# Kernel optimization log

Hardware: AMD Instinct MI355X
Metric: run time of the kernel (lower is better)

Reference implementation:

```python
import jax, jax.numpy as jnp
import numpy as np

BETA = 10.0


def _read_buffer(alpha, B, s_b, pop):
    # alpha: [b], B: [b,S,H], s_b: [b,S]. Closed form of the saturating
    # sequential read: cumsum after i steps = min(prefix_sum(s_b)_i, alpha),
    # so weight_i = min(P_i, alpha) - min(P_{i-1}, alpha).
    P = jnp.cumsum(s_b, axis=1)
    Pc = jnp.minimum(P, alpha[:, None])
    w = Pc - jnp.concatenate([jnp.zeros_like(Pc[:, :1]), Pc[:, :-1]], axis=1)
    vec = jnp.einsum('bs,bsh->bh', w, B)
    return vec, (s_b - w if pop else s_b)


def _read_stack(alpha, V, s, pop):
    # V: [M,b,H], s: [M,b]; smaller index = closer to stack top (unused slots
    # above the top have s==0 and contribute nothing).
    P = jnp.cumsum(s, axis=0)                 # [M,b]
    a = alpha[None, :]
    Pc1 = jnp.minimum(P, a)                   # saturate at alpha (first read)
    Pc2 = jnp.minimum(P, 1.0 + a)             # saturate at 1+alpha (both reads)
    z = jnp.zeros_like(P[:1])
    w1 = Pc1 - jnp.concatenate([z, Pc1[:-1]], axis=0)
    wt = Pc2 - jnp.concatenate([z, Pc2[:-1]], axis=0)
    w2 = wt - w1
    v1 = jnp.einsum('mb,mbh->bh', w1, V)
    v2 = jnp.einsum('mb,mbh->bh', w2, V)
    return v1, v2, (s - wt if pop else s)


def _forward(x, emb_table, lstm_wih, lstm_whh, lstm_bih, lstm_bhh,
             alpha_w, alpha_b, tree_left_w, tree_left_b, tree_right_w,
             tree_right_b, l0_w, l0_b, l1_w, l1_b, l2_w, l2_b):
    b, S = x.shape
    H = emb_table.shape[1]
    time = 2 * S
    M = 1 + 2 * time                          # max stack depth
    B = emb_table[x]                          # [b,S,H]
    s_b0 = (x > 0).astype(jnp.float32)
    V0 = jnp.zeros((M, b, H), jnp.float32)    # initial sentinel at M-1 (zeros)
    s0 = jnp.zeros((M, b), jnp.float32)
    h0 = jnp.zeros((b, H), jnp.float32)
    c0 = jnp.zeros((b, H), jnp.float32)
    ones_b = jnp.ones((b,), jnp.float32)

    def step(carry, t):
        s_b, V, s, h, c = carry
        n = 1 + 2 * t                         # current number of stack items
        x_b, _ = _read_buffer(ones_b, B, s_b, False)
        x1, x2, _ = _read_stack(ones_b, V, s, False)
        xt = jnp.concatenate([x_b, x1, x2], axis=1)
        # LSTMCell (torch gate order i,f,g,o)
        g = xt @ lstm_wih.T + lstm_bih + h @ lstm_whh.T + lstm_bhh
        gi, gf, gg, go = jnp.split(g, 4, axis=1)
        c = jax.nn.sigmoid(gf) * c + jax.nn.sigmoid(gi) * jnp.tanh(gg)
        h = jax.nn.sigmoid(go) * jnp.tanh(c)
        alphas = jax.nn.softmax(BETA * (h @ alpha_w.T + alpha_b), axis=1)
        a_r, a_s = alphas[:, 0], alphas[:, 1]
        # reduce: pop ~2 items, treeLSTM, push result with strength alpha_r
        r1, r2, s = _read_stack(a_r, V, s, True)
        tg = r1 @ tree_left_w.T + tree_left_b + r2 @ tree_right_w.T + tree_right_b
        ta, ti, tf1, tf2, to = jnp.split(tg, 5, axis=1)
        ct = jnp.tanh(ta) * jax.nn.sigmoid(ti) + jax.nn.sigmoid(tf1) * r1 + jax.nn.sigmoid(tf2) * r2
        ht = jax.nn.sigmoid(to) * jnp.tanh(ct)
        idx = M - (n + 1)
        V = V.at[idx].set(ht)
        s = s.at[idx].set(a_r)
        # shift: pop from buffer with strength alpha_s, push onto stack
        buf, s_b = _read_buffer(a_s, B, s_b, True)
        idx2 = M - (n + 2)
        V = V.at[idx2].set(buf)
        s = s.at[idx2].set(a_s)
        return (s_b, V, s, h, c), None

    carry, _ = jax.lax.scan(jax.checkpoint(step), (s_b0, V0, s0, h0, c0),
                            jnp.arange(time))
    s_b, V, s, h, c = carry
    x1, _, _ = _read_stack(ones_b, V, s, False)
    # MLP head
    y = jax.nn.relu(x1 @ l0_w.T + l0_b)
    y = jax.nn.relu(y @ l1_w.T + l1_b)
    return y @ l2_w.T + l2_b


def setup_inputs() -> dict:
    key = jax.random.key(0)
    ks = jax.random.split(key, 12)
    b, S, H, V, MLP, C = 64, 48, 256, 50257, 1024, 3
    sc = 0.05
    return {
        'x': jax.random.randint(ks[0], (b, S), 0, V, dtype=jnp.int32).astype(jnp.int64),
        'emb_table': jax.random.normal(ks[1], (V, H), jnp.float32) * sc,
        'lstm_wih': jax.random.normal(ks[2], (4 * H, 3 * H), jnp.float32) * sc,
        'lstm_whh': jax.random.normal(ks[3], (4 * H, H), jnp.float32) * sc,
        'lstm_bih': jnp.zeros((4 * H,), jnp.float32),
        'lstm_bhh': jnp.zeros((4 * H,), jnp.float32),
        'alpha_w': jax.random.normal(ks[4], (2, H), jnp.float32) * sc,
        'alpha_b': jnp.zeros((2,), jnp.float32),
        'tree_left_w': jax.random.normal(ks[5], (5 * H, H), jnp.float32) * sc,
        'tree_left_b': jnp.zeros((5 * H,), jnp.float32),
        'tree_right_w': jax.random.normal(ks[6], (5 * H, H), jnp.float32) * sc,
        'tree_right_b': jnp.zeros((5 * H,), jnp.float32),
        'l0_w': jax.random.normal(ks[7], (MLP, H), jnp.float32) * sc,
        'l0_b': jnp.zeros((MLP,), jnp.float32),
        'l1_w': jax.random.normal(ks[8], (MLP, MLP), jnp.float32) * sc,
        'l1_b': jnp.zeros((MLP,), jnp.float32),
        'l2_w': jax.random.normal(ks[9], (C, MLP), jnp.float32) * sc,
        'l2_b': jnp.zeros((C,), jnp.float32),
    }


def reference(x, emb_table, lstm_wih, lstm_whh, lstm_bih, lstm_bhh, alpha_w,
              alpha_b, tree_left_w, tree_left_b, tree_right_w, tree_right_b,
              l0_w, l0_b, l1_w, l1_b, l2_w, l2_b):
    return _forward(x, emb_table, lstm_wih, lstm_whh, lstm_bih, lstm_bhh,
                    alpha_w, alpha_b, tree_left_w, tree_left_b, tree_right_w,
                    tree_right_b, l0_w, l0_b, l1_w, l1_b, l2_w, l2_b)
```

## Files before the change

kernel.cpp:

```cpp
#include <hip/hip_runtime.h>
#include <math.h>

#define NBLK 512
#define NTHR 512

typedef float vf4 __attribute__((ext_vector_type(4)));

namespace spinn {

constexpr int Ss = 48, Hh = 256, TT = 96, Mm = 193, H3 = 768, MLPD = 1024;

__device__ __forceinline__ float sigf(float x) { return 1.0f / (1.0f + expf(-x)); }

#define FMA4(acc, a, b)                         \
    {                                           \
        acc.x = fmaf((a).x, (b).x, acc.x);      \
        acc.y = fmaf((a).y, (b).y, acc.y);      \
        acc.z = fmaf((a).z, (b).z, acc.z);      \
        acc.w = fmaf((a).w, (b).w, acc.w);      \
    }

__device__ __forceinline__ void st_co(float* p, float v) {
    asm volatile("global_store_dword %0, %1, off sc0 sc1" :: "v"(p), "v"(v) : "memory");
}
__device__ __forceinline__ void ld_co_v4_1(const vf4* p0, vf4& r0) {
    asm volatile("global_load_dwordx4 %0, %1, off sc0 sc1\n\t"
                 "s_waitcnt vmcnt(0)"
                 : "=&v"(r0) : "v"(p0) : "memory");
}
__device__ __forceinline__ void ld_co_f1x4(const float* p0, const float* p1, const float* p2,
                                           const float* p3, float& r0, float& r1, float& r2, float& r3) {
    asm volatile("global_load_dword %0, %4, off sc0 sc1\n\t"
                 "global_load_dword %1, %5, off sc0 sc1\n\t"
                 "global_load_dword %2, %6, off sc0 sc1\n\t"
                 "global_load_dword %3, %7, off sc0 sc1\n\t"
                 "s_waitcnt vmcnt(0)"
                 : "=&v"(r0), "=&v"(r1), "=&v"(r2), "=&v"(r3)
                 : "v"(p0), "v"(p1), "v"(p2), "v"(p3) : "memory");
}
__device__ __forceinline__ unsigned ld_co_u32(const unsigned* p) {
    unsigned r;
    asm volatile("global_load_dword %0, %1, off sc0 sc1\n\t"
                 "s_waitcnt vmcnt(0)"
                 : "=&v"(r) : "v"(p) : "memory");
    return r;
}

__device__ __forceinline__ void gbar(unsigned* cnt, unsigned tgt) {
    asm volatile("s_waitcnt vmcnt(0)" ::: "memory");
    __syncthreads();
    if (threadIdx.x == 0) {
        unsigned one = 1u;
        asm volatile("global_atomic_add %0, %1, off" :: "v"(cnt), "v"(one) : "memory");
        while (ld_co_u32(cnt) < tgt) __builtin_amdgcn_s_sleep(1);
    }
    __syncthreads();
}

__device__ __forceinline__ float wave_iscan(float v, int lane) {
    #pragma unroll
    for (int off = 1; off < 64; off <<= 1) {
        float u = __shfl_up(v, off, 64);
        if (lane >= off) v += u;
    }
    return v;
}
__device__ __forceinline__ float wred64(float v) {
    #pragma unroll
    for (int off = 1; off < 64; off <<= 1) v += __shfl_xor(v, off, 64);
    return v;
}
__device__ __forceinline__ float wred_ms(float v) {
    v += __shfl_xor(v, 16, 64);
    v += __shfl_xor(v, 32, 64);
    return v;
}

}

using namespace spinn;

__global__ void __launch_bounds__(NTHR, 2) spinn_kernel(
    const int* __restrict__ x, const float* __restrict__ emb,
    const float* __restrict__ wih, const float* __restrict__ whh,
    const float* __restrict__ bih, const float* __restrict__ bhh,
    const float* __restrict__ aw, const float* __restrict__ ab,
    const float* __restrict__ tlw, const float* __restrict__ tlb,
    const float* __restrict__ trw, const float* __restrict__ trb,
    const float* __restrict__ l0w, const float* __restrict__ l0b,
    const float* __restrict__ l1w, const float* __restrict__ l1b,
    const float* __restrict__ l2w, const float* __restrict__ l2b,
    float* __restrict__ out, float* __restrict__ wsf, unsigned* __restrict__ bar)
{
    const int tid  = threadIdx.x;
    const int bid  = blockIdx.x;
    const int ep   = bid >> 4;
    const int q    = bid & 15;
    const int db   = q * 16;
    const int e0   = ep * 2;
    const int wave = tid >> 6;
    const int lane = tid & 63;
    const int ms   = lane >> 4;
    const int dl   = lane & 15;

    unsigned* cnt = bar + ep * 32;
    unsigned barnum = 0;

    float* XTg = wsf;
    float* Hbg = XTg + 64 * H3;
    float* R1g = Hbg + 64 * Hh;
    float* R2g = R1g + 64 * Hh;
    float* Y0g = R2g + 64 * Hh;
    float* Y1g = Y0g + 64 * MLPD;

    __shared__ float s_V[2 * 196 * 16];
    __shared__ float s_B[2 * Ss * 16];
    __shared__ float s_xt[2 * H3];
    __shared__ float s_h[2 * 256];
    __shared__ float s_c[32];
    __shared__ float s_g[128];
    __shared__ float s_tg[160];
    __shared__ float s_r1[2 * 256], s_r2[2 * 256];
    __shared__ float s_s[2 * 208];
    __shared__ float sw1[2 * 208], sw2[2 * 208];
    __shared__ float pw1[2 * 208], pw2[2 * 208];
    __shared__ float s_sb[2 * Ss], s_wb[2 * Ss], s_wbe[2 * Ss];
    __shared__ float s_bias[64];
    __shared__ float s_tbias[80];

    float* s_y = s_V;

    {
        if (tid < 384) {
            int el = tid / 192, r = tid % 192;
            int s = r >> 2, j = r & 3;
            int tok = x[(e0 + el) * Ss + s];
            ((vf4*)s_B)[el * 192 + s * 4 + j] = ((const vf4*)emb)[(size_t)tok * 64 + q * 4 + j];
        }
        if (tid < 2 * Ss) {
            int el = tid / Ss, s = tid % Ss;
            s_sb[tid] = (x[(e0 + el) * Ss + s] > 0) ? 1.0f : 0.0f;
        }
        for (int i = tid; i < 2 * 208; i += NTHR) s_s[i] = 0.0f;
        for (int i = tid; i < 2 * 256; i += NTHR) s_h[i] = 0.0f;
        if (tid < 32) s_c[tid] = 0.0f;
        if (tid < 64) {
            int row = (tid >> 4) * Hh + db + (tid & 15);
            s_bias[tid] = bih[row] + bhh[row];
        }
        if (tid < 80) {
            int row = (tid >> 4) * Hh + db + (tid & 15);
            s_tbias[tid] = tlb[row] + trb[row];
        }
        for (int i = tid; i < 2 * 196 * 16; i += NTHR) s_V[i] = 0.0f;
        __syncthreads();
        if (wave < 2) {
            int el = wave;
            float sbv = (lane < Ss) ? s_sb[el * Ss + lane] : 0.0f;
            float P = wave_iscan(sbv, lane);
            float wbe = fminf(P, 1.0f) - fminf(P - sbv, 1.0f);
            if (lane < Ss) s_wbe[el * Ss + lane] = wbe;
            float axb = 0.0f;
            #pragma unroll
            for (int j = 0; j < 12; j++) {
                int s = ms * 12 + j;
                axb = fmaf(s_wbe[el * Ss + s], s_B[el * 768 + s * 16 + dl], axb);
            }
            axb = wred_ms(axb);
            if (lane < 16) {
                float* xte = XTg + (size_t)(e0 + el) * H3;
                st_co(xte + db + dl, axb);
                st_co(xte + 256 + db + dl, 0.0f);
                st_co(xte + 512 + db + dl, 0.0f);
            }
        }
    }
    gbar(cnt, ++barnum * 16);

    for (int t = 0; t < TT; t++) {
        const int idx  = 191 - 2 * t;
        const int idx2 = idx - 1;

        {
            if (tid < 384) {
                int el = tid / 192, r = tid % 192;
                vf4 v;
                ld_co_v4_1((const vf4*)XTg + (size_t)(e0 + el) * 192 + r, v);
                ((vf4*)s_xt)[el * 192 + r] = v;
            }
            __syncthreads();
            const vf4* sxt4 = (const vf4*)s_xt;
            const vf4* sh4  = (const vf4*)s_h;
            vf4 xa0 = sxt4[lane], xa1 = sxt4[64 + lane], xa2 = sxt4[128 + lane];
            vf4 xb0 = sxt4[192 + lane], xb1 = sxt4[256 + lane], xb2 = sxt4[320 + lane];
            vf4 ha = sh4[lane], hb = sh4[64 + lane];
            #pragma unroll 2
            for (int p = 0; p < 8; p++) {
                int r = wave * 8 + p;
                int row = ((r >> 4) << 8) + db + (r & 15);
                const vf4* w  = (const vf4*)wih + (size_t)row * 192;
                const vf4* wh = (const vf4*)whh + (size_t)row * 64;
                vf4 w0 = w[lane], w1 = w[64 + lane], w2 = w[128 + lane], w3 = wh[lane];
                vf4 aa = {0.f, 0.f, 0.f, 0.f}, ab_ = {0.f, 0.f, 0.f, 0.f};
                FMA4(aa, w0, xa0); FMA4(aa, w1, xa1); FMA4(aa, w2, xa2); FMA4(aa, w3, ha);
                FMA4(ab_, w0, xb0); FMA4(ab_, w1, xb1); FMA4(ab_, w2, xb2); FMA4(ab_, w3, hb);
                float sa = wred64(aa.x + aa.y + aa.z + aa.w);
                float sb = wred64(ab_.x + ab_.y + ab_.z + ab_.w);
                if (lane == 0) {
                    s_g[r] = sa + s_bias[r];
                    s_g[64 + r] = sb + s_bias[r];
                }
            }
            __syncthreads();
            if (tid < 32) {
                int el = tid >> 4, d = tid & 15;
                int base = el * 64;
                float gi = s_g[base + d], gf = s_g[base + 16 + d];
                float gg = s_g[base + 32 + d], go = s_g[base + 48 + d];
                float cv = sigf(gf) * s_c[tid] + sigf(gi) * tanhf(gg);
                s_c[tid] = cv;
                float hv = sigf(go) * tanhf(cv);
                st_co(Hbg + (size_t)(e0 + el) * Hh + db + d, hv);
            }
        }
        gbar(cnt, ++barnum * 16);

        {
            if (wave < 4) {
                int el = wave & 1;
                int e = e0 + el;
                float h0, h1, h2, h3;
                const float* hb = Hbg + (size_t)e * Hh + lane;
                ld_co_f1x4(hb, hb + 64, hb + 128, hb + 192, h0, h1, h2, h3);
                if (wave < 2) {
                    s_h[el * 256 + lane] = h0;       s_h[el * 256 + 64 + lane] = h1;
                    s_h[el * 256 + 128 + lane] = h2; s_h[el * 256 + 192 + lane] = h3;
                }
                float lg0 = h0 * aw[lane] + h1 * aw[64 + lane] + h2 * aw[128 + lane] + h3 * aw[192 + lane];
                float lg1 = h0 * aw[256 + lane] + h1 * aw[320 + lane] + h2 * aw[384 + lane] + h3 * aw[448 + lane];
                lg0 = wred64(lg0) + ab[0];
                lg1 = wred64(lg1) + ab[1];
                float a_r = 1.0f / (1.0f + expf(10.0f * (lg1 - lg0)));
                float a_s = 1.0f / (1.0f + expf(10.0f * (lg0 - lg1)));

                if (wave < 2) {
                    int m0 = lane * 4;
                    int sb_ = el * 208;
                    float v0 = (m0     < Mm) ? s_s[sb_ + m0]     : 0.0f;
                    float v1 = (m0 + 1 < Mm) ? s_s[sb_ + m0 + 1] : 0.0f;
                    float v2 = (m0 + 2 < Mm) ? s_s[sb_ + m0 + 2] : 0.0f;
                    float v3 = (m0 + 3 < Mm) ? s_s[sb_ + m0 + 3] : 0.0f;
                    float c1 = v0 + v1, c2 = c1 + v2, c3 = c2 + v3;
                    float inc = c3;
                    #pragma unroll
                    for (int off = 1; off < 64; off <<= 1) {
                        float u = __shfl_up(inc, off, 64);
                        if (lane >= off) inc += u;
                    }
                    float ex = inc - c3;
                    float Pv[4]  = {ex + v0, ex + c1, ex + c2, ex + c3};
                    float Pp[4]  = {ex, ex + v0, ex + c1, ex + c2};
                    float vv_[4] = {v0, v1, v2, v3};
                    float sn[4];
                    #pragma unroll
                    for (int i = 0; i < 4; i++) {
                        int m = m0 + i;
                        float w1 = fminf(Pv[i], a_r) - fminf(Pp[i], a_r);
                        float wt = fminf(Pv[i], 1.0f + a_r) - fminf(Pp[i], 1.0f + a_r);
                        float s2 = vv_[i] - wt;
                        if (m == idx)  s2 = a_r;
                        if (m == idx2) s2 = a_s;
                        sn[i] = s2;
                        if (m < Mm) {
                            sw1[sb_ + m] = w1;
                            sw2[sb_ + m] = wt - w1;
                            s_s[sb_ + m] = s2;
                        } else if (m < 208) {
                            sw1[sb_ + m] = 0.0f; sw2[sb_ + m] = 0.0f;
                        }
                    }
                    float d1 = sn[0] + sn[1], d2 = d1 + sn[2], d3 = d2 + sn[3];
                    float inc2 = d3;
                    #pragma unroll
                    for (int off = 1; off < 64; off <<= 1) {
                        float u = __shfl_up(inc2, off, 64);
                        if (lane >= off) inc2 += u;
                    }
                    float ex2 = inc2 - d3;
                    float Qv[4] = {ex2 + sn[0], ex2 + d1, ex2 + d2, ex2 + d3};
                    float Qp[4] = {ex2, ex2 + sn[0], ex2 + d1, ex2 + d2};
                    #pragma unroll
                    for (int i = 0; i < 4; i++) {
                        int m = m0 + i;
                        if (m < Mm) {
                            float w1e = fminf(Qv[i], 1.0f) - fminf(Qp[i], 1.0f);
                            pw1[sb_ + m] = w1e;
                            pw2[sb_ + m] = (fminf(Qv[i], 2.0f) - fminf(Qp[i], 2.0f)) - w1e;
                        } else if (m < 208) {
                            pw1[sb_ + m] = 0.0f; pw2[sb_ + m] = 0.0f;
                        }
                    }
                } else {
                    float sbv = (lane < Ss) ? s_sb[el * Ss + lane] : 0.0f;
                    float Pb = wave_iscan(sbv, lane);
                    float wb = fminf(Pb, a_s) - fminf(Pb - sbv, a_s);
                    float sbn = sbv - wb;
                    float Pb2 = wave_iscan(sbn, lane);
                    float wbe = fminf(Pb2, 1.0f) - fminf(Pb2 - sbn, 1.0f);
                    if (lane < Ss) {
                        s_sb[el * Ss + lane] = sbn;
                        s_wb[el * Ss + lane] = wb;
                        s_wbe[el * Ss + lane] = wbe;
                    }
                    float abf = 0.0f, axb = 0.0f;
                    #pragma unroll
                    for (int j = 0; j < 12; j++) {
                        int s = ms * 12 + j;
                        float be = s_B[el * 768 + s * 16 + dl];
                        abf = fmaf(s_wb[el * Ss + s], be, abf);
                        axb = fmaf(s_wbe[el * Ss + s], be, axb);
                    }
                    abf = wred_ms(abf); axb = wred_ms(axb);
                    if (lane < 16) {
                        s_V[el * 3136 + idx2 * 16 + dl] = abf;
                        st_co(XTg + (size_t)e * H3 + db + dl, axb);
                    }
                }
            }
            __syncthreads();
            if (wave < 2) {
                int el = wave, e = e0 + el;
                float a1 = 0.0f, a2 = 0.0f;
                #pragma unroll 7
                for (int k = 0; k < 49; k++) {
                    int m = ms * 49 + k;
                    float vv = s_V[el * 3136 + m * 16 + dl];
                    a1 = fmaf(sw1[el * 208 + m], vv, a1);
                    a2 = fmaf(sw2[el * 208 + m], vv, a2);
                }
                a1 = wred_ms(a1); a2 = wred_ms(a2);
                if (lane < 16) {
                    st_co(R1g + (size_t)e * Hh + db + dl, a1);
                    st_co(R2g + (size_t)e * Hh + db + dl, a2);
                }
            }
        }
        gbar(cnt, ++barnum * 16);

        {
            if (tid < 256) {
                int part = tid >> 6, r = tid & 63;
                int el = part >> 1;
                vf4 v;
                if (part & 1) {
                    ld_co_v4_1((const vf4*)R2g + (size_t)(e0 + el) * 64 + r, v);
                    ((vf4*)s_r2)[el * 64 + r] = v;
                } else {
                    ld_co_v4_1((const vf4*)R1g + (size_t)(e0 + el) * 64 + r, v);
                    ((vf4*)s_r1)[el * 64 + r] = v;
                }
            }
            __syncthreads();
            const vf4* sr14 = (const vf4*)s_r1;
            const vf4* sr24 = (const vf4*)s_r2;
            vf4 r1a = sr14[lane], r2a = sr24[lane];
            vf4 r1b = sr14[64 + lane], r2b = sr24[64 + lane];
            #pragma unroll 2
            for (int p = 0; p < 10; p++) {
                int r = wave * 10 + p;
                int row = ((r >> 4) << 8) + db + (r & 15);
                const vf4* wl = (const vf4*)tlw + (size_t)row * 64;
                const vf4* wr = (const vf4*)trw + (size_t)row * 64;
                vf4 u = wl[lane], v = wr[lane];
                vf4 aa = {0.f, 0.f, 0.f, 0.f}, ab_ = {0.f, 0.f, 0.f, 0.f};
                FMA4(aa, u, r1a); FMA4(aa, v, r2a);
                FMA4(ab_, u, r1b); FMA4(ab_, v, r2b);
                float sa = wred64(aa.x + aa.y + aa.z + aa.w);
                float sb = wred64(ab_.x + ab_.y + ab_.z + ab_.w);
                if (lane == 0) {
                    s_tg[r] = sa + s_tbias[r];
                    s_tg[80 + r] = sb + s_tbias[r];
                }
            }
            __syncthreads();
            if (tid < 32) {
                int el = tid >> 4, d = tid & 15;
                int base = el * 80;
                float ta  = s_tg[base + d];
                float ti  = s_tg[base + 16 + d];
                float tf1 = s_tg[base + 32 + d];
                float tf2 = s_tg[base + 48 + d];
                float to  = s_tg[base + 64 + d];
                float r1d = s_r1[el * 256 + db + d];
                float r2d = s_r2[el * 256 + db + d];
                float ct = tanhf(ta) * sigf(ti) + sigf(tf1) * r1d + sigf(tf2) * r2d;
                s_V[el * 3136 + idx * 16 + d] = sigf(to) * tanhf(ct);
            }
            __syncthreads();
            if (wave < 2) {
                int el = wave, e = e0 + el;
                float x1 = 0.0f, x2 = 0.0f;
                #pragma unroll 7
                for (int k = 0; k < 49; k++) {
                    int m = ms * 49 + k;
                    float vv = s_V[el * 3136 + m * 16 + dl];
                    x1 = fmaf(pw1[el * 208 + m], vv, x1);
                    x2 = fmaf(pw2[el * 208 + m], vv, x2);
                }
                x1 = wred_ms(x1); x2 = wred_ms(x2);
                if (lane < 16) {
                    st_co(XTg + (size_t)e * H3 + 256 + db + dl, x1);
                    st_co(XTg + (size_t)e * H3 + 512 + db + dl, x2);
                }
            }
        }
        gbar(cnt, ++barnum * 16);
    }

    {
        if (tid < 128) {
            int el = tid >> 6, r = tid & 63;
            vf4 v;
            ld_co_v4_1((const vf4*)XTg + (size_t)(e0 + el) * 192 + 64 + r, v);
            ((vf4*)s_y)[el * 64 + r] = v;
        }
        __syncthreads();
        vf4 xina = ((const vf4*)s_y)[lane];
        vf4 xinb = ((const vf4*)s_y)[64 + lane];
        #pragma unroll 2
        for (int p = 0; p < 8; p++) {
            int row = q * 64 + wave * 8 + p;
            vf4 wv = ((const vf4*)l0w)[(size_t)row * 64 + lane];
            vf4 aa = {0.f, 0.f, 0.f, 0.f}, ab_ = {0.f, 0.f, 0.f, 0.f};
            FMA4(aa, wv, xina); FMA4(ab_, wv, xinb);
            float sa = wred64(aa.x + aa.y + aa.z + aa.w);
            float sb = wred64(ab_.x + ab_.y + ab_.z + ab_.w);
            if (lane == 0) {
                st_co(Y0g + (size_t)e0 * MLPD + row, fmaxf(sa + l0b[row], 0.0f));
                st_co(Y0g + (size_t)(e0 + 1) * MLPD + row, fmaxf(sb + l0b[row], 0.0f));
            }
        }
    }
    gbar(cnt, ++barnum * 16);
    {
        {
            int el = tid >> 8, r = tid & 255;
            vf4 v;
            ld_co_v4_1((const vf4*)Y0g + (size_t)(e0 + el) * 256 + r, v);
            ((vf4*)s_y)[el * 256 + r] = v;
        }
        __syncthreads();
        const vf4* sy4 = (const vf4*)s_y;
        vf4 ya0 = sy4[lane], ya1 = sy4[64 + lane], ya2 = sy4[128 + lane], ya3 = sy4[192 + lane];
        vf4 yb0 = sy4[256 + lane], yb1 = sy4[320 + lane], yb2 = sy4[384 + lane], yb3 = sy4[448 + lane];
        #pragma unroll 2
        for (int p = 0; p < 8; p++) {
            int row = q * 64 + wave * 8 + p;
            const vf4* w = (const vf4*)l1w + (size_t)row * 256;
            vf4 w0 = w[lane], w1 = w[64 + lane], w2 = w[128 + lane], w3 = w[192 + lane];
            vf4 aa = {0.f, 0.f, 0.f, 0.f}, ab_ = {0.f, 0.f, 0.f, 0.f};
            FMA4(aa, w0, ya0); FMA4(aa, w1, ya1); FMA4(aa, w2, ya2); FMA4(aa, w3, ya3);
            FMA4(ab_, w0, yb0); FMA4(ab_, w1, yb1); FMA4(ab_, w2, yb2); FMA4(ab_, w3, yb3);
            float sa = wred64(aa.x + aa.y + aa.z + aa.w);
            float sb = wred64(ab_.x + ab_.y + ab_.z + ab_.w);
            if (lane == 0) {
                st_co(Y1g + (size_t)e0 * MLPD + row, fmaxf(sa + l1b[row], 0.0f));
                st_co(Y1g + (size_t)(e0 + 1) * MLPD + row, fmaxf(sb + l1b[row], 0.0f));
            }
        }
    }
    gbar(cnt, ++barnum * 16);
    if (q < 2) {
        int e = e0 + q;
        if (tid < 256) {
            vf4 v;
            ld_co_v4_1((const vf4*)Y1g + (size_t)e * 256 + tid, v);
            ((vf4*)s_y)[tid] = v;
        }
        __syncthreads();
        if (tid < 192) {
            int r = tid >> 6;
            const vf4* w = (const vf4*)l2w + (size_t)r * 256;
            vf4 acc = {0.f, 0.f, 0.f, 0.f};
            #pragma unroll
            for (int j = 0; j < 4; j++) {
                vf4 wv = w[lane + j * 64], yv = ((const vf4*)s_y)[lane + j * 64];
                FMA4(acc, wv, yv);
            }
            float sv = wred64(acc.x + acc.y + acc.z + acc.w);
            if (lane == 0) out[e * 3 + r] = sv + l2b[r];
        }
    }
}

extern "C" void kernel_launch(void* const* d_in, const int* in_sizes, int n_in,
                              void* d_out, int out_size, void* d_ws, size_t ws_size,
                              hipStream_t stream) {
    (void)in_sizes; (void)n_in; (void)out_size; (void)ws_size;
    (void)hipMemsetAsync(d_ws, 0, 4096, stream);

    const int*   x_   = (const int*)d_in[0];
    const float* emb  = (const float*)d_in[1];
    const float* wih  = (const float*)d_in[2];
    const float* whh  = (const float*)d_in[3];
    const float* bih  = (const float*)d_in[4];
    const float* bhh  = (const float*)d_in[5];
    const float* aw   = (const float*)d_in[6];
    const float* ab   = (const float*)d_in[7];
    const float* tlw  = (const float*)d_in[8];
    const float* tlb  = (const float*)d_in[9];
    const float* trw  = (const float*)d_in[10];
    const float* trb  = (const float*)d_in[11];
    const float* l0w  = (const float*)d_in[12];
    const float* l0b  = (const float*)d_in[13];
    const float* l1w  = (const float*)d_in[14];
    const float* l1b  = (const float*)d_in[15];
    const float* l2w  = (const float*)d_in[16];
    const float* l2b  = (const float*)d_in[17];

    float* wsf = (float*)((char*)d_ws + 4096);
    unsigned* bar = (unsigned*)d_ws;

    spinn_kernel<<<dim3(NBLK), dim3(NTHR), 0, stream>>>(
        x_, emb, wih, whh, bih, bhh, aw, ab, tlw, tlb, trw, trb,
        l0w, l0b, l1w, l1b, l2w, l2b, (float*)d_out, wsf, bar);
}
```

Measured before the change: 3.500 ms.

## Split hidden dimension across twice as many smaller blocks per example pair

Doubles the number of cooperating blocks per example pair, from 16 to 32, and halves threads per block from 512 to 256. Each block now owns 8 hidden units instead of 16, which halves per-block weight streaming and stack-read work per step and lets more blocks sit on each CU. In exchange, every grid barrier must now wait for twice as many participants, raising synchronization latency on each of the roughly 290 per-step barriers. Reductions and shared-memory layouts are reindexed to match the narrower slice.

Result: slower. 3.893 ms (+11.2%).

```diff
diff --git a/kernel.cpp b/kernel.cpp
--- a/kernel.cpp
+++ b/kernel.cpp
@@ -1,14 +1,15 @@
 #include <hip/hip_runtime.h>
 #include <math.h>
 
-#define NBLK 512
-#define NTHR 512
+#define NBLK 1024
+#define NTHR 256
 
 typedef float vf4 __attribute__((ext_vector_type(4)));
 
 namespace spinn {
 
 constexpr int Ss = 48, Hh = 256, TT = 96, Mm = 193, H3 = 768, MLPD = 1024;
+constexpr int Mp = 200;
 
 __device__ __forceinline__ float sigf(float x) { return 1.0f / (1.0f + expf(-x)); }
 
@@ -70,7 +71,8 @@
     for (int off = 1; off < 64; off <<= 1) v += __shfl_xor(v, off, 64);
     return v;
 }
-__device__ __forceinline__ float wred_ms(float v) {
+__device__ __forceinline__ float wred_mg(float v) {
+    v += __shfl_xor(v, 8, 64);
     v += __shfl_xor(v, 16, 64);
     v += __shfl_xor(v, 32, 64);
     return v;
@@ -80,7 +82,7 @@
 
 using namespace spinn;
 
-__global__ void __launch_bounds__(NTHR, 2) spinn_kernel(
+__global__ void __launch_bounds__(NTHR, 4) spinn_kernel(
     const int* __restrict__ x, const float* __restrict__ emb,
     const float* __restrict__ wih, const float* __restrict__ whh,
     const float* __restrict__ bih, const float* __restrict__ bhh,
@@ -94,14 +96,14 @@
 {
     const int tid  = threadIdx.x;
     const int bid  = blockIdx.x;
-    const int ep   = bid >> 4;
-    const int q    = bid & 15;
-    const int db   = q * 16;
+    const int ep   = bid >> 5;
+    const int q8   = bid & 31;
+    const int db   = q8 * 8;
     const int e0   = ep * 2;
     const int wave = tid >> 6;
     const int lane = tid & 63;
-    const int ms   = lane >> 4;
-    const int dl   = lane & 15;
+    const int mg   = lane >> 3;
+    const int dl8  = lane & 7;
 
     unsigned* cnt = bar + ep * 32;
     unsigned barnum = 0;
@@ -113,46 +115,46 @@
     float* Y0g = R2g + 64 * Hh;
     float* Y1g = Y0g + 64 * MLPD;
 
-    __shared__ float s_V[2 * 196 * 16];
-    __shared__ float s_B[2 * Ss * 16];
+    __shared__ float s_V[2 * Mp * 8];
+    __shared__ float s_B[2 * Ss * 8];
     __shared__ float s_xt[2 * H3];
     __shared__ float s_h[2 * 256];
-    __shared__ float s_c[32];
-    __shared__ float s_g[128];
-    __shared__ float s_tg[160];
+    __shared__ float s_c[16];
+    __shared__ float s_g[64];
+    __shared__ float s_tg[80];
     __shared__ float s_r1[2 * 256], s_r2[2 * 256];
-    __shared__ float s_s[2 * 208];
-    __shared__ float sw1[2 * 208], sw2[2 * 208];
-    __shared__ float pw1[2 * 208], pw2[2 * 208];
+    __shared__ float s_s[2 * Mp];
+    __shared__ float sw1[2 * Mp], sw2[2 * Mp];
+    __shared__ float pw1[2 * Mp], pw2[2 * Mp];
     __shared__ float s_sb[2 * Ss], s_wb[2 * Ss], s_wbe[2 * Ss];
-    __shared__ float s_bias[64];
-    __shared__ float s_tbias[80];
+    __shared__ float s_bias[32];
+    __shared__ float s_tbias[40];
 
     float* s_y = s_V;
 
     {
-        if (tid < 384) {
-            int el = tid / 192, r = tid % 192;
-            int s = r >> 2, j = r & 3;
+        if (tid < 192) {
+            int el = tid / 96, r = tid % 96;
+            int s = r >> 1, j = r & 1;
             int tok = x[(e0 + el) * Ss + s];
-            ((vf4*)s_B)[el * 192 + s * 4 + j] = ((const vf4*)emb)[(size_t)tok * 64 + q * 4 + j];
+            ((vf4*)s_B)[el * 96 + s * 2 + j] = ((const vf4*)emb)[(size_t)tok * 64 + q8 * 2 + j];
         }
         if (tid < 2 * Ss) {
             int el = tid / Ss, s = tid % Ss;
             s_sb[tid] = (x[(e0 + el) * Ss + s] > 0) ? 1.0f : 0.0f;
         }
-        for (int i = tid; i < 2 * 208; i += NTHR) s_s[i] = 0.0f;
+        for (int i = tid; i < 2 * Mp; i += NTHR) s_s[i] = 0.0f;
         for (int i = tid; i < 2 * 256; i += NTHR) s_h[i] = 0.0f;
-        if (tid < 32) s_c[tid] = 0.0f;
-        if (tid < 64) {
-            int row = (tid >> 4) * Hh + db + (tid & 15);
+        if (tid < 16) s_c[tid] = 0.0f;
+        if (tid < 32) {
+            int row = (tid >> 3) * Hh + db + (tid & 7);
             s_bias[tid] = bih[row] + bhh[row];
         }
-        if (tid < 80) {
-            int row = (tid >> 4) * Hh + db + (tid & 15);
+        if (tid < 40) {
+            int row = (tid >> 3) * Hh + db + (tid & 7);
             s_tbias[tid] = tlb[row] + trb[row];
         }
-        for (int i = tid; i < 2 * 196 * 16; i += NTHR) s_V[i] = 0.0f;
+        for (int i = tid; i < 2 * Mp * 8; i += NTHR) s_V[i] = 0.0f;
         __syncthreads();
         if (wave < 2) {
             int el = wave;
@@ -162,28 +164,28 @@
             if (lane < Ss) s_wbe[el * Ss + lane] = wbe;
             float axb = 0.0f;
             #pragma unroll
-            for (int j = 0; j < 12; j++) {
-                int s = ms * 12 + j;
-                axb = fmaf(s_wbe[el * Ss + s], s_B[el * 768 + s * 16 + dl], axb);
-            }
-            axb = wred_ms(axb);
-            if (lane < 16) {
+            for (int j = 0; j < 6; j++) {
+                int s = mg * 6 + j;
+                axb = fmaf(s_wbe[el * Ss + s], s_B[el * 384 + s * 8 + dl8], axb);
+            }
+            axb = wred_mg(axb);
+            if (lane < 8) {
                 float* xte = XTg + (size_t)(e0 + el) * H3;
-                st_co(xte + db + dl, axb);
-                st_co(xte + 256 + db + dl, 0.0f);
-                st_co(xte + 512 + db + dl, 0.0f);
-            }
-        }
-    }
-    gbar(cnt, ++barnum * 16);
+                st_co(xte + db + dl8, axb);
+                st_co(xte + 256 + db + dl8, 0.0f);
+                st_co(xte + 512 + db + dl8, 0.0f);
+            }
+        }
+    }
+    gbar(cnt, ++barnum * 32);
 
     for (int t = 0; t < TT; t++) {
         const int idx  = 191 - 2 * t;
         const int idx2 = idx - 1;
 
         {
-            if (tid < 384) {
-                int el = tid / 192, r = tid % 192;
+            for (int i = tid; i < 384; i += NTHR) {
+                int el = i / 192, r = i % 192;
                 vf4 v;
                 ld_co_v4_1((const vf4*)XTg + (size_t)(e0 + el) * 192 + r, v);
                 ((vf4*)s_xt)[el * 192 + r] = v;
@@ -197,7 +199,7 @@
             #pragma unroll 2
             for (int p = 0; p < 8; p++) {
                 int r = wave * 8 + p;
-                int row = ((r >> 4) << 8) + db + (r & 15);
+                int row = ((r >> 3) << 8) + db + (r & 7);
                 const vf4* w  = (const vf4*)wih + (size_t)row * 192;
                 const vf4* wh = (const vf4*)whh + (size_t)row * 64;
                 vf4 w0 = w[lane], w1 = w[64 + lane], w2 = w[128 + lane], w3 = wh[lane];
@@ -208,147 +210,144 @@
                 float sb = wred64(ab_.x + ab_.y + ab_.z + ab_.w);
                 if (lane == 0) {
                     s_g[r] = sa + s_bias[r];
-                    s_g[64 + r] = sb + s_bias[r];
+                    s_g[32 + r] = sb + s_bias[r];
                 }
             }
             __syncthreads();
-            if (tid < 32) {
-                int el = tid >> 4, d = tid & 15;
-                int base = el * 64;
-                float gi = s_g[base + d], gf = s_g[base + 16 + d];
-                float gg = s_g[base + 32 + d], go = s_g[base + 48 + d];
+            if (tid < 16) {
+                int el = tid >> 3, d = tid & 7;
+                int base = el * 32;
+                float gi = s_g[base + d], gf = s_g[base + 8 + d];
+                float gg = s_g[base + 16 + d], go = s_g[base + 24 + d];
                 float cv = sigf(gf) * s_c[tid] + sigf(gi) * tanhf(gg);
                 s_c[tid] = cv;
                 float hv = sigf(go) * tanhf(cv);
                 st_co(Hbg + (size_t)(e0 + el) * Hh + db + d, hv);
             }
         }
-        gbar(cnt, ++barnum * 16);
+        gbar(cnt, ++barnum * 32);
 
         {
-            if (wave < 4) {
-                int el = wave & 1;
-                int e = e0 + el;
-                float h0, h1, h2, h3;
-                const float* hb = Hbg + (size_t)e * Hh + lane;
-                ld_co_f1x4(hb, hb + 64, hb + 128, hb + 192, h0, h1, h2, h3);
-                if (wave < 2) {
-                    s_h[el * 256 + lane] = h0;       s_h[el * 256 + 64 + lane] = h1;
-                    s_h[el * 256 + 128 + lane] = h2; s_h[el * 256 + 192 + lane] = h3;
-                }
-                float lg0 = h0 * aw[lane] + h1 * aw[64 + lane] + h2 * aw[128 + lane] + h3 * aw[192 + lane];
-                float lg1 = h0 * aw[256 + lane] + h1 * aw[320 + lane] + h2 * aw[384 + lane] + h3 * aw[448 + lane];
-                lg0 = wred64(lg0) + ab[0];
-                lg1 = wred64(lg1) + ab[1];
-                float a_r = 1.0f / (1.0f + expf(10.0f * (lg1 - lg0)));
-                float a_s = 1.0f / (1.0f + expf(10.0f * (lg0 - lg1)));
-
-                if (wave < 2) {
-                    int m0 = lane * 4;
-                    int sb_ = el * 208;
-                    float v0 = (m0     < Mm) ? s_s[sb_ + m0]     : 0.0f;
-                    float v1 = (m0 + 1 < Mm) ? s_s[sb_ + m0 + 1] : 0.0f;
-                    float v2 = (m0 + 2 < Mm) ? s_s[sb_ + m0 + 2] : 0.0f;
-                    float v3 = (m0 + 3 < Mm) ? s_s[sb_ + m0 + 3] : 0.0f;
-                    float c1 = v0 + v1, c2 = c1 + v2, c3 = c2 + v3;
-                    float inc = c3;
-                    #pragma unroll
-                    for (int off = 1; off < 64; off <<= 1) {
-                        float u = __shfl_up(inc, off, 64);
-                        if (lane >= off) inc += u;
+            int el = wave & 1;
+            int e = e0 + el;
+            float h0, h1, h2, h3;
+            const float* hb = Hbg + (size_t)e * Hh + lane;
+            ld_co_f1x4(hb, hb + 64, hb + 128, hb + 192, h0, h1, h2, h3);
+            if (wave < 2) {
+                s_h[el * 256 + lane] = h0;       s_h[el * 256 + 64 + lane] = h1;
+                s_h[el * 256 + 128 + lane] = h2; s_h[el * 256 + 192 + lane] = h3;
+            }
+            float lg0 = h0 * aw[lane] + h1 * aw[64 + lane] + h2 * aw[128 + lane] + h3 * aw[192 + lane];
+            float lg1 = h0 * aw[256 + lane] + h1 * aw[320 + lane] + h2 * aw[384 + lane] + h3 * aw[448 + lane];
+            lg0 = wred64(lg0) + ab[0];
+            lg1 = wred64(lg1) + ab[1];
+            float a_r = 1.0f / (1.0f + expf(10.0f * (lg1 - lg0)));
+            float a_s = 1.0f / (1.0f + expf(10.0f * (lg0 - lg1)));
+
+            if (wave < 2) {
+                int m0 = lane * 4;
+                int sb_ = el * Mp;
+                float v0 = (m0     < Mm) ? s_s[sb_ + m0]     : 0.0f;
+                float v1 = (m0 + 1 < Mm) ? s_s[sb_ + m0 + 1] : 0.0f;
+                float v2 = (m0 + 2 < Mm) ? s_s[sb_ + m0 + 2] : 0.0f;
+                float v3 = (m0 + 3 < Mm) ? s_s[sb_ + m0 + 3] : 0.0f;
+                float c1 = v0 + v1, c2 = c1 + v2, c3 = c2 + v3;
+                float inc = c3;
+                #pragma unroll
+                for (int off = 1; off < 64; off <<= 1) {
+                    float u = __shfl_up(inc, off, 64);
+                    if (lane >= off) inc += u;
+                }
+                float ex = inc - c3;
+                float Pv[4]  = {ex + v0, ex + c1, ex + c2, ex + c3};
+                float Pp[4]  = {ex, ex + v0, ex + c1, ex + c2};
+                float vv_[4] = {v0, v1, v2, v3};
+                float sn[4];
+                #pragma unroll
+                for (int i = 0; i < 4; i++) {
+                    int m = m0 + i;
+                    float w1 = fminf(Pv[i], a_r) - fminf(Pp[i], a_r);
+                    float wt = fminf(Pv[i], 1.0f + a_r) - fminf(Pp[i], 1.0f + a_r);
+                    float s2 = vv_[i] - wt;
+                    if (m == idx)  s2 = a_r;
+                    if (m == idx2) s2 = a_s;
+                    sn[i] = s2;
+                    if (m < Mm) {
+                        sw1[sb_ + m] = w1;
+                        sw2[sb_ + m] = wt - w1;
+                        s_s[sb_ + m] = s2;
+                    } else if (m < Mp) {
+                        sw1[sb_ + m] = 0.0f; sw2[sb_ + m] = 0.0f;
                     }
-                    float ex = inc - c3;
-                    float Pv[4]  = {ex + v0, ex + c1, ex + c2, ex + c3};
-                    float Pp[4]  = {ex, ex + v0, ex + c1, ex + c2};
-                    float vv_[4] = {v0, v1, v2, v3};
-                    float sn[4];
-                    #pragma unroll
-                    for (int i = 0; i < 4; i++) {
-                        int m = m0 + i;
-                        float w1 = fminf(Pv[i], a_r) - fminf(Pp[i], a_r);
-                        float wt = fminf(Pv[i], 1.0f + a_r) - fminf(Pp[i], 1.0f + a_r);
-                        float s2 = vv_[i] - wt;
-                        if (m == idx)  s2 = a_r;
-                        if (m == idx2) s2 = a_s;
-                        sn[i] = s2;
-                        if (m < Mm) {
-                            sw1[sb_ + m] = w1;
-                            sw2[sb_ + m] = wt - w1;
-                            s_s[sb_ + m] = s2;
-                        } else if (m < 208) {
-                            sw1[sb_ + m] = 0.0f; sw2[sb_ + m] = 0.0f;
-                        }
+                }
+                float d1 = sn[0] + sn[1], d2 = d1 + sn[2], d3 = d2 + sn[3];
+                float inc2 = d3;
+                #pragma unroll
+                for (int off = 1; off < 64; off <<= 1) {
+                    float u = __shfl_up(inc2, off, 64);
+                    if (lane >= off) inc2 += u;
+                }
+                float ex2 = inc2 - d3;
+                float Qv[4] = {ex2 + sn[0], ex2 + d1, ex2 + d2, ex2 + d3};
+                float Qp[4] = {ex2, ex2 + sn[0], ex2 + d1, ex2 + d2};
+                #pragma unroll
+                for (int i = 0; i < 4; i++) {
+                    int m = m0 + i;
+                    if (m < Mm) {
+                        float w1e = fminf(Qv[i], 1.0f) - fminf(Qp[i], 1.0f);
+                        pw1[sb_ + m] = w1e;
+                        pw2[sb_ + m] = (fminf(Qv[i], 2.0f) - fminf(Qp[i], 2.0f)) - w1e;
+                    } else if (m < Mp) {
+                        pw1[sb_ + m] = 0.0f; pw2[sb_ + m] = 0.0f;
                     }
-                    float d1 = sn[0] + sn[1], d2 = d1 + sn[2], d3 = d2 + sn[3];
-                    float inc2 = d3;
-                    #pragma unroll
-                    for (int off = 1; off < 64; off <<= 1) {
-                        float u = __shfl_up(inc2, off, 64);
-                        if (lane >= off) inc2 += u;
-                    }
-                    float ex2 = inc2 - d3;
-                    float Qv[4] = {ex2 + sn[0], ex2 + d1, ex2 + d2, ex2 + d3};
-                    float Qp[4] = {ex2, ex2 + sn[0], ex2 + d1, ex2 + d2};
-                    #pragma unroll
-                    for (int i = 0; i < 4; i++) {
-                        int m = m0 + i;
-                        if (m < Mm) {
-                            float w1e = fminf(Qv[i], 1.0f) - fminf(Qp[i], 1.0f);
-                            pw1[sb_ + m] = w1e;
-                            pw2[sb_ + m] = (fminf(Qv[i], 2.0f) - fminf(Qp[i], 2.0f)) - w1e;
-                        } else if (m < 208) {
-                            pw1[sb_ + m] = 0.0f; pw2[sb_ + m] = 0.0f;
-                        }
-                    }
-                } else {
-                    float sbv = (lane < Ss) ? s_sb[el * Ss + lane] : 0.0f;
-                    float Pb = wave_iscan(sbv, lane);
-                    float wb = fminf(Pb, a_s) - fminf(Pb - sbv, a_s);
-                    float sbn = sbv - wb;
-                    float Pb2 = wave_iscan(sbn, lane);
-                    float wbe = fminf(Pb2, 1.0f) - fminf(Pb2 - sbn, 1.0f);
-                    if (lane < Ss) {
-                        s_sb[el * Ss + lane] = sbn;
-                        s_wb[el * Ss + lane] = wb;
-                        s_wbe[el * Ss + lane] = wbe;
-                    }
-                    float abf = 0.0f, axb = 0.0f;
-                    #pragma unroll
-                    for (int j = 0; j < 12; j++) {
-                        int s = ms * 12 + j;
-                        float be = s_B[el * 768 + s * 16 + dl];
-                        abf = fmaf(s_wb[el * Ss + s], be, abf);
-                        axb = fmaf(s_wbe[el * Ss + s], be, axb);
-                    }
-                    abf = wred_ms(abf); axb = wred_ms(axb);
-                    if (lane < 16) {
-                        s_V[el * 3136 + idx2 * 16 + dl] = abf;
-                        st_co(XTg + (size_t)e * H3 + db + dl, axb);
-                    }
+                }
+            } else {
+                float sbv = (lane < Ss) ? s_sb[el * Ss + lane] : 0.0f;
+                float Pb = wave_iscan(sbv, lane);
+                float wb = fminf(Pb, a_s) - fminf(Pb - sbv, a_s);
+                float sbn = sbv - wb;
+                float Pb2 = wave_iscan(sbn, lane);
+                float wbe = fminf(Pb2, 1.0f) - fminf(Pb2 - sbn, 1.0f);
+                if (lane < Ss) {
+                    s_sb[el * Ss + lane] = sbn;
+                    s_wb[el * Ss + lane] = wb;
+                    s_wbe[el * Ss + lane] = wbe;
+                }
+                float abf = 0.0f, axb = 0.0f;
+                #pragma unroll
+                for (int j = 0; j < 6; j++) {
+                    int s = mg * 6 + j;
+                    float be = s_B[el * 384 + s * 8 + dl8];
+                    abf = fmaf(s_wb[el * Ss + s], be, abf);
+                    axb = fmaf(s_wbe[el * Ss + s], be, axb);
+                }
+                abf = wred_mg(abf); axb = wred_mg(axb);
+                if (lane < 8) {
+                    s_V[el * (Mp * 8) + idx2 * 8 + dl8] = abf;
+                    st_co(XTg + (size_t)e * H3 + db + dl8, axb);
                 }
             }
             __syncthreads();
             if (wave < 2) {
-                int el = wave, e = e0 + el;
                 float a1 = 0.0f, a2 = 0.0f;
-                #pragma unroll 7
-                for (int k = 0; k < 49; k++) {
-                    int m = ms * 49 + k;
-                    float vv = s_V[el * 3136 + m * 16 + dl];
-                    a1 = fmaf(sw1[el * 208 + m], vv, a1);
-                    a2 = fmaf(sw2[el * 208 + m], vv, a2);
-                }
-                a1 = wred_ms(a1); a2 = wred_ms(a2);
-                if (lane < 16) {
-                    st_co(R1g + (size_t)e * Hh + db + dl, a1);
-                    st_co(R2g + (size_t)e * Hh + db + dl, a2);
-                }
-            }
-        }
-        gbar(cnt, ++barnum * 16);
+                #pragma unroll 5
+                for (int k = 0; k < 25; k++) {
+                    int m = mg * 25 + k;
+                    float vv = s_V[el * (Mp * 8) + m * 8 + dl8];
+                    a1 = fmaf(sw1[el * Mp + m], vv, a1);
+                    a2 = fmaf(sw2[el * Mp + m], vv, a2);
+                }
+                a1 = wred_mg(a1); a2 = wred_mg(a2);
+                if (lane < 8) {
+                    st_co(R1g + (size_t)e * Hh + db + dl8, a1);
+                    st_co(R2g + (size_t)e * Hh + db + dl8, a2);
+                }
+            }
+        }
+        gbar(cnt, ++barnum * 32);
 
         {
-            if (tid < 256) {
+            {
                 int part = tid >> 6, r = tid & 63;
                 int el = part >> 1;
                 vf4 v;
@@ -368,7 +367,7 @@
             #pragma unroll 2
             for (int p = 0; p < 10; p++) {
                 int r = wave * 10 + p;
-                int row = ((r >> 4) << 8) + db + (r & 15);
+                int row = ((r >> 3) << 8) + db + (r & 7);
                 const vf4* wl = (const vf4*)tlw + (size_t)row * 64;
                 const vf4* wr = (const vf4*)trw + (size_t)row * 64;
                 vf4 u = wl[lane], v = wr[lane];
@@ -379,42 +378,42 @@
                 float sb = wred64(ab_.x + ab_.y + ab_.z + ab_.w);
                 if (lane == 0) {
                     s_tg[r] = sa + s_tbias[r];
-                    s_tg[80 + r] = sb + s_tbias[r];
+                    s_tg[40 + r] = sb + s_tbias[r];
                 }
             }
             __syncthreads();
-            if (tid < 32) {
-                int el = tid >> 4, d = tid & 15;
-                int base = el * 80;
+            if (tid < 16) {
+                int el = tid >> 3, d = tid & 7;
+                int base = el * 40;
                 float ta  = s_tg[base + d];
-                float ti  = s_tg[base + 16 + d];
-                float tf1 = s_tg[base + 32 + d];
-                float tf2 = s_tg[base + 48 + d];
-                float to  = s_tg[base + 64 + d];
+                float ti  = s_tg[base + 8 + d];
+                float tf1 = s_tg[base + 16 + d];
+                float tf2 = s_tg[base + 24 + d];
+                float to  = s_tg[base + 32 + d];
                 float r1d = s_r1[el * 256 + db + d];
                 float r2d = s_r2[el * 256 + db + d];
                 float ct = tanhf(ta) * sigf(ti) + sigf(tf1) * r1d + sigf(tf2) * r2d;
-                s_V[el * 3136 + idx * 16 + d] = sigf(to) * tanhf(ct);
+                s_V[el * (Mp * 8) + idx * 8 + d] = sigf(to) * tanhf(ct);
             }
             __syncthreads();
             if (wave < 2) {
                 int el = wave, e = e0 + el;
                 float x1 = 0.0f, x2 = 0.0f;
-                #pragma unroll 7
-                for (int k = 0; k < 49; k++) {
-                    int m = ms * 49 + k;
-                    float vv = s_V[el * 3136 + m * 16 + dl];
-                    x1 = fmaf(pw1[el * 208 + m], vv, x1);
-                    x2 = fmaf(pw2[el * 208 + m], vv, x2);
-                }
-                x1 = wred_ms(x1); x2 = wred_ms(x2);
-                if (lane < 16) {
-                    st_co(XTg + (size_t)e * H3 + 256 + db + dl, x1);
-                    st_co(XTg + (size_t)e * H3 + 512 + db + dl, x2);
-                }
-            }
-        }
-        gbar(cnt, ++barnum * 16);
+                #pragma unroll 5
+                for (int k = 0; k < 25; k++) {
+                    int m = mg * 25 + k;
+                    float vv = s_V[el * (Mp * 8) + m * 8 + dl8];
+                    x1 = fmaf(pw1[el * Mp + m], vv, x1);
+                    x2 = fmaf(pw2[el * Mp + m], vv, x2);
+                }
+                x1 = wred_mg(x1); x2 = wred_mg(x2);
+                if (lane < 8) {
+                    st_co(XTg + (size_t)e * H3 + 256 + db + dl8, x1);
+                    st_co(XTg + (size_t)e * H3 + 512 + db + dl8, x2);
+                }
+            }
+        }
+        gbar(cnt, ++barnum * 32);
     }
 
     {
@@ -429,7 +428,7 @@
         vf4 xinb = ((const vf4*)s_y)[64 + lane];
         #pragma unroll 2
         for (int p = 0; p < 8; p++) {
-            int row = q * 64 + wave * 8 + p;
+            int row = q8 * 32 + wave * 8 + p;
             vf4 wv = ((const vf4*)l0w)[(size_t)row * 64 + lane];
             vf4 aa = {0.f, 0.f, 0.f, 0.f}, ab_ = {0.f, 0.f, 0.f, 0.f};
             FMA4(aa, wv, xina); FMA4(ab_, wv, xinb);
@@ -441,10 +440,10 @@
             }
         }
     }
-    gbar(cnt, ++barnum * 16);
+    gbar(cnt, ++barnum * 32);
     {
-        {
-            int el = tid >> 8, r = tid & 255;
+        for (int i = tid; i < 512; i += NTHR) {
+            int el = i >> 8, r = i & 255;
             vf4 v;
             ld_co_v4_1((const vf4*)Y0g + (size_t)(e0 + el) * 256 + r, v);
             ((vf4*)s_y)[el * 256 + r] = v;
@@ -455,7 +454,7 @@
         vf4 yb0 = sy4[256 + lane], yb1 = sy4[320 + lane], yb2 = sy4[384 + lane], yb3 = sy4[448 + lane];
         #pragma unroll 2
         for (int p = 0; p < 8; p++) {
-            int row = q * 64 + wave * 8 + p;
+            int row = q8 * 32 + wave * 8 + p;
             const vf4* w = (const vf4*)l1w + (size_t)row * 256;
             vf4 w0 = w[lane], w1 = w[64 + lane], w2 = w[128 + lane], w3 = w[192 + lane];
             vf4 aa = {0.f, 0.f, 0.f, 0.f}, ab_ = {0.f, 0.f, 0.f, 0.f};
@@ -469,10 +468,10 @@
             }
         }
     }
-    gbar(cnt, ++barnum * 16);
-    if (q < 2) {
-        int e = e0 + q;
-        if (tid < 256) {
+    gbar(cnt, ++barnum * 32);
+    if (q8 < 2) {
+        int e = e0 + q8;
+        {
             vf4 v;
             ld_co_v4_1((const vf4*)Y1g + (size_t)e * 256 + tid, v);
             ((vf4*)s_y)[tid] = v;
```
